# Kernel tuning notes

Measured on AMD Instinct MI355X. Metric: run time of the kernel, lower is better.

The kernel has to match this reference:

```python
import jax, jax.numpy as jnp
import numpy as np

NUM_HEADS = 8
EPS = 1e-12  # torch F.normalize eps

def _conv(x, w, padding, groups=1):
    return jax.lax.conv_general_dilated(
        x, w, window_strides=(1, 1), padding=padding,
        dimension_numbers=('NCHW', 'OIHW', 'NCHW'),
        feature_group_count=groups)

def setup_inputs() -> dict:
    key = jax.random.key(0)
    ks = jax.random.split(key, 5)
    b, dim, h, w = 8, 192, 128, 128
    kv = jax.random.normal(ks[0], (b, dim, h, w), dtype=jnp.float32)
    q = jax.random.normal(ks[1], (b, dim, h, w), dtype=jnp.float32)
    qkv1_w = jax.random.normal(ks[2], (2 * dim, dim, 1, 1), dtype=jnp.float32) * (1.0 / np.sqrt(dim))
    qkv2_w = jax.random.normal(ks[3], (2 * dim, 1, 3, 3), dtype=jnp.float32) * (1.0 / 3.0)
    proj_w = jax.random.normal(ks[4], (dim, dim, 1, 1), dtype=jnp.float32) * (1.0 / np.sqrt(dim))
    scale = jnp.ones((NUM_HEADS, 1, 1), dtype=jnp.float32)
    return {"kv": kv, "q": q, "qkv1_w": qkv1_w, "qkv2_w": qkv2_w,
            "proj_w": proj_w, "scale": scale}

def reference(kv, q, qkv1_w, qkv2_w, proj_w, scale):
    b, c, h, w = kv.shape
    head = NUM_HEADS
    cd = c // head  # channels per head
    hw = h * w
    # 1x1 conv dim -> 2*dim, then 3x3 depthwise conv (groups = 2*dim)
    kv_f = _conv(kv, qkv1_w, padding='VALID')
    kv_f = _conv(kv_f, qkv2_w, padding=((1, 1), (1, 1)), groups=2 * c)
    k, v = jnp.split(kv_f, 2, axis=1)
    # rearrange to [b, head, c, hw]
    qh = q.reshape(b, head, cd, hw)
    kh = k.reshape(b, head, cd, hw)
    vh = v.reshape(b, head, cd, hw)
    # L2-normalize along spatial dim (torch F.normalize semantics)
    qh = qh / jnp.maximum(jnp.linalg.norm(qh, axis=-1, keepdims=True), EPS)
    kh = kh / jnp.maximum(jnp.linalg.norm(kh, axis=-1, keepdims=True), EPS)
    # channel attention: [b, head, c, c]
    attn = jnp.einsum('bhcn,bhdn->bhcd', qh, kh) * scale  # scale broadcasts [head,1,1]
    attn = jax.nn.softmax(attn, axis=-1)
    out = jnp.einsum('bhcd,bhdn->bhcn', attn, vh)  # [b, head, c, hw]
    out = out.reshape(b, c, h, w)
    out = _conv(out, proj_w, padding='VALID')
    return out
```

## Files before the change

kernel.cpp:

```cpp
#include <hip/hip_runtime.h>
#include <hip/hip_bf16.h>

#define HW 16384
#define DIM 192
#define DIM2 384
#define NB 8
#define HEADS 8
#define CD 24
#define NSPLIT 64

typedef float f32x4 __attribute__((ext_vector_type(4)));
typedef short bf16x8 __attribute__((ext_vector_type(8)));
typedef short s16x4 __attribute__((ext_vector_type(4)));

__device__ __forceinline__ short f2bf(float f) {
    __hip_bfloat16 h = __float2bfloat16(f);
    return *reinterpret_cast<short*>(&h);
}
__device__ __forceinline__ float bf2f(short s) {
    __hip_bfloat16 h = *reinterpret_cast<__hip_bfloat16*>(&s);
    return __bfloat162float(h);
}

__global__ __launch_bounds__(256)
void prep_w1(const float* __restrict__ w1, short* __restrict__ wb1)
{
    int idx = blockIdx.x * 256 + threadIdx.x;
    if (idx >= 9216) return;
    int mi = idx / 384, rem = idx % 384;
    int c = rem >> 6, l = rem & 63;
    int oc = mi * 16 + (l & 15);
    int kb = c * 32 + (l >> 4) * 8;
    const float* src = w1 + (long)oc * DIM + kb;
    float4 v0 = *reinterpret_cast<const float4*>(src);
    float4 v1 = *reinterpret_cast<const float4*>(src + 4);
    bf16x8 o;
    o[0]=f2bf(v0.x); o[1]=f2bf(v0.y); o[2]=f2bf(v0.z); o[3]=f2bf(v0.w);
    o[4]=f2bf(v1.x); o[5]=f2bf(v1.y); o[6]=f2bf(v1.z); o[7]=f2bf(v1.w);
    *reinterpret_cast<bf16x8*>(wb1 + (long)idx * 8) = o;
}

template<int NOCT, bool B_F32, bool PER_BATCH_A, bool OUT_F32>
__global__ __launch_bounds__(256, 2)
void gemm_k192(const short* __restrict__ Ab, const void* __restrict__ Bg,
               void* __restrict__ Cg, long bstrideB, long bstrideC)
{
    __shared__ short lds[128 * 200];
    __shared__ float eps[4][16 * 36];
    const int tid  = threadIdx.x;
    const int lane = tid & 63;
    const int wave = tid >> 6;
    const int pxbase = blockIdx.x * 256;
    const int b    = blockIdx.y;

    const int row  = lane & 15;
    const int kgrp = lane >> 4;
    const short* A0 = Ab + (PER_BATCH_A ? (long)b * NOCT * 3072 : 0);

    bf16x8 aA[6], aB[6];
    auto loadA = [&](bf16x8* dst, int mi) {
#pragma unroll
        for (int c = 0; c < 6; c++)
            dst[c] = *reinterpret_cast<const bf16x8*>(
                &A0[((long)(mi * 6 + c) * 64 + lane) * 8]);
    };

    const int q  = tid & 31;
    const int kl = tid >> 5;
    f32x4 stf[6][4];
    s16x4 sth[6][4];
    auto SLOAD = [&](int px0) {
        if constexpr (B_F32) {
            const float* src = (const float*)Bg + (long)b * bstrideB + px0 + q * 4;
#pragma unroll
            for (int j = 0; j < 6; j++)
#pragma unroll
                for (int e = 0; e < 4; e++)
                    stf[j][e] = __builtin_nontemporal_load(
                        reinterpret_cast<const f32x4*>(src + (long)(32 * j + 4 * kl + e) * HW));
        } else {
            const short* src = (const short*)Bg + (long)b * bstrideB + px0 + q * 4;
#pragma unroll
            for (int j = 0; j < 6; j++)
#pragma unroll
                for (int e = 0; e < 4; e++)
                    sth[j][e] = __builtin_nontemporal_load(
                        reinterpret_cast<const s16x4*>(src + (long)(32 * j + 4 * kl + e) * HW));
        }
    };
    auto SWRITE = [&]() {
        const int goff = (((kl >> 1) ^ (q & 3)) << 3) + (kl & 1) * 4;
#pragma unroll
        for (int j = 0; j < 6; j++) {
#pragma unroll
            for (int i = 0; i < 4; i++) {
                s16x4 t;
                if constexpr (B_F32)
                    t = (s16x4){f2bf(stf[j][0][i]), f2bf(stf[j][1][i]),
                                f2bf(stf[j][2][i]), f2bf(stf[j][3][i])};
                else
                    t = (s16x4){sth[j][0][i], sth[j][1][i], sth[j][2][i], sth[j][3][i]};
                *(s16x4*)&lds[(q * 4 + i) * 200 + 32 * j + goff] = t;
            }
        }
    };

    bf16x8 bv[2][6];
    auto HOIST = [&]() {
        const int bro = wave * 32 + row;
        const int sgr = (row >> 2) & 3;
#pragma unroll
        for (int c = 0; c < 6; c++) {
            bv[0][c] = *(const bf16x8*)&lds[bro * 200 + c * 32 + ((kgrp ^ sgr) << 3)];
            bv[1][c] = *(const bf16x8*)&lds[(bro + 16) * 200 + c * 32 + ((kgrp ^ sgr) << 3)];
        }
    };

    const int ocl = lane >> 2;
    float* ep = &eps[wave][0];
    auto computeStore = [&](const bf16x8* a, int mi, int px0) {
        f32x4 acc0 = (f32x4){0.f, 0.f, 0.f, 0.f};
        f32x4 acc1 = (f32x4){0.f, 0.f, 0.f, 0.f};
#pragma unroll
        for (int c = 0; c < 6; c++) {
            acc0 = __builtin_amdgcn_mfma_f32_16x16x32_bf16(a[c], bv[0][c], acc0, 0, 0, 0);
            acc1 = __builtin_amdgcn_mfma_f32_16x16x32_bf16(a[c], bv[1][c], acc1, 0, 0, 0);
        }
#pragma unroll
        for (int r = 0; r < 4; r++) {
            ep[(kgrp * 4 + r) * 36 + row]      = acc0[r];
            ep[(kgrp * 4 + r) * 36 + 16 + row] = acc1[r];
        }
#pragma unroll
        for (int t = 0; t < 2; t++) {
            const int pxq = (lane & 3) + t * 4;
            f32x4 vv = *reinterpret_cast<const f32x4*>(&ep[ocl * 36 + pxq * 4]);
            long off = (long)b * bstrideC + (long)(mi * 16 + ocl) * HW
                     + px0 + wave * 32 + pxq * 4;
            if constexpr (OUT_F32) {
                __builtin_nontemporal_store(vv, reinterpret_cast<f32x4*>((float*)Cg + off));
            } else {
                *reinterpret_cast<s16x4*>((short*)Cg + off) =
                    (s16x4){f2bf(vv[0]), f2bf(vv[1]), f2bf(vv[2]), f2bf(vv[3])};
            }
        }
    };
    auto COMPUTE = [&](int px0) {
        for (int mi = 0; mi < NOCT; mi += 2) {
            loadA(aB, mi + 1);
            computeStore(aA, mi, px0);
            if (mi + 2 < NOCT) loadA(aA, mi + 2);
            computeStore(aB, mi + 1, px0);
        }
    };

    loadA(aA, 0);
    SLOAD(pxbase);
    SWRITE();
    __syncthreads();
    HOIST();
    __syncthreads();
    SLOAD(pxbase + 128);
    COMPUTE(pxbase);
    loadA(aA, 0);
    SWRITE();
    __syncthreads();
    HOIST();
    COMPUTE(pxbase + 128);
}

__global__ __launch_bounds__(256)
void dwconv_sumsq(const short* __restrict__ in, const float* __restrict__ w2,
                  short* __restrict__ outp, float* __restrict__ kss)
{
    __shared__ float red[4];
    const long bgc = blockIdx.x;
    const int  gc  = (int)(bgc % DIM2);
    const int  b   = (int)(bgc / DIM2);
    const int  tid = threadIdx.x;
    const int  tx  = tid & 15;
    const int  ty  = tid >> 4;
    const int  lane = tid & 63;
    const int  x0 = tx * 8;
    const int  y0 = ty * 8;
    const short* src = in + (bgc << 14);
    short* dst = outp + (bgc << 14);

    float w[9];
#pragma unroll
    for (int i = 0; i < 9; i++) w[i] = w2[gc * 9 + i];

    float r0[10], r1[10], r2[10];
    auto loadRow = [&](float* r, int y) {
        if ((unsigned)y > 127u) {
#pragma unroll
            for (int i = 0; i < 10; i++) r[i] = 0.f;
            return;
        }
        bf16x8 v = *reinterpret_cast<const bf16x8*>(&src[y * 128 + x0]);
#pragma unroll
        for (int i = 0; i < 8; i++) r[i + 1] = bf2f(v[i]);
        float left  = __shfl(r[8], lane - 1);
        float right = __shfl(r[1], lane + 1);
        r[0] = (tx == 0)  ? 0.f : left;
        r[9] = (tx == 15) ? 0.f : right;
    };

    loadRow(r0, y0 - 1);
    loadRow(r1, y0);
    float ssq = 0.f;
#pragma unroll
    for (int k = 0; k < 8; k++) {
        const int yy = y0 + k;
        loadRow(r2, yy + 1);
        bf16x8 o;
#pragma unroll
        for (int j = 0; j < 8; j++) {
            float s = r0[j] * w[0] + r0[j + 1] * w[1] + r0[j + 2] * w[2]
                    + r1[j] * w[3] + r1[j + 1] * w[4] + r1[j + 2] * w[5]
                    + r2[j] * w[6] + r2[j + 1] * w[7] + r2[j + 2] * w[8];
            o[j] = f2bf(s);
            ssq += s * s;
        }
        *reinterpret_cast<bf16x8*>(&dst[yy * 128 + x0]) = o;
#pragma unroll
        for (int i = 0; i < 10; i++) { r0[i] = r1[i]; r1[i] = r2[i]; }
    }

    for (int o = 32; o; o >>= 1) ssq += __shfl_xor(ssq, o);
    if ((tid & 63) == 0) red[tid >> 6] = ssq;
    __syncthreads();
    if (gc < DIM && tid == 0)
        kss[b * DIM + gc] = red[0] + red[1] + red[2] + red[3];
}

__global__ __launch_bounds__(64)
void qk_mfma(const float* __restrict__ q, const short* __restrict__ kvb,
             float* __restrict__ part, float* __restrict__ pssq)
{
    const int split = blockIdx.x;
    const int bh    = blockIdx.y;
    const int b = bh >> 3, h = bh & 7;
    const int lane = threadIdx.x;
    const int row = lane & 15;
    const int kg  = (lane >> 4) * 8;
    const int CHUNK = HW / NSPLIT;

    const int qr1 = min(h * CD + 16 + row, DIM - 1);
    const float* q0 = q + ((long)b * DIM + h * CD + row) * HW + split * CHUNK + kg;
    const float* q1 = q + ((long)b * DIM + qr1) * HW + split * CHUNK + kg;
    const short* k0 = kvb + ((long)b * DIM2 + h * CD + row) * HW + split * CHUNK + kg;
    const short* k1 = k0 + 16L * HW;

    f32x4 acc[2][2];
#pragma unroll
    for (int m = 0; m < 2; m++)
#pragma unroll
        for (int n = 0; n < 2; n++) acc[m][n] = (f32x4){0.f, 0.f, 0.f, 0.f};
    float ssq0 = 0.f, ssq1 = 0.f;

#pragma unroll
    for (int s = 0; s < CHUNK / 32; s++) {
        const int px = s * 32;
        float4 qa = *reinterpret_cast<const float4*>(q0 + px);
        float4 qb = *reinterpret_cast<const float4*>(q0 + px + 4);
        float4 qc = *reinterpret_cast<const float4*>(q1 + px);
        float4 qd = *reinterpret_cast<const float4*>(q1 + px + 4);
        bf16x8 b0 = *reinterpret_cast<const bf16x8*>(k0 + px);
        bf16x8 b1 = *reinterpret_cast<const bf16x8*>(k1 + px);
        ssq0 += qa.x*qa.x + qa.y*qa.y + qa.z*qa.z + qa.w*qa.w
              + qb.x*qb.x + qb.y*qb.y + qb.z*qb.z + qb.w*qb.w;
        ssq1 += qc.x*qc.x + qc.y*qc.y + qc.z*qc.z + qc.w*qc.w
              + qd.x*qd.x + qd.y*qd.y + qd.z*qd.z + qd.w*qd.w;
        bf16x8 a0, a1;
        a0[0]=f2bf(qa.x); a0[1]=f2bf(qa.y); a0[2]=f2bf(qa.z); a0[3]=f2bf(qa.w);
        a0[4]=f2bf(qb.x); a0[5]=f2bf(qb.y); a0[6]=f2bf(qb.z); a0[7]=f2bf(qb.w);
        a1[0]=f2bf(qc.x); a1[1]=f2bf(qc.y); a1[2]=f2bf(qc.z); a1[3]=f2bf(qc.w);
        a1[4]=f2bf(qd.x); a1[5]=f2bf(qd.y); a1[6]=f2bf(qd.z); a1[7]=f2bf(qd.w);
        acc[0][0] = __builtin_amdgcn_mfma_f32_16x16x32_bf16(a0, b0, acc[0][0], 0, 0, 0);
        acc[0][1] = __builtin_amdgcn_mfma_f32_16x16x32_bf16(a0, b1, acc[0][1], 0, 0, 0);
        acc[1][0] = __builtin_amdgcn_mfma_f32_16x16x32_bf16(a1, b0, acc[1][0], 0, 0, 0);
        acc[1][1] = __builtin_amdgcn_mfma_f32_16x16x32_bf16(a1, b1, acc[1][1], 0, 0, 0);
    }

    ssq0 += __shfl_xor(ssq0, 16); ssq0 += __shfl_xor(ssq0, 32);
    ssq1 += __shfl_xor(ssq1, 16); ssq1 += __shfl_xor(ssq1, 32);

    float* pd = part + ((long)split * 64 + bh) * 576;
#pragma unroll
    for (int m = 0; m < 2; m++)
#pragma unroll
        for (int n = 0; n < 2; n++)
#pragma unroll
            for (int r = 0; r < 4; r++) {
                int c = m * 16 + (lane >> 4) * 4 + r;
                int d = n * 16 + row;
                if (c < CD && d < CD) pd[c * CD + d] = acc[m][n][r];
            }
    if (lane < 16) {
        float* ps = pssq + ((long)split * 64 + bh) * 32;
        ps[lane]      = ssq0;
        ps[16 + lane] = ssq1;
    }
}

__global__ __launch_bounds__(64)
void softmax_kernel(const float* __restrict__ part, const float* __restrict__ pssq,
                    const float* __restrict__ kss, const float* __restrict__ scale,
                    float* __restrict__ prob)
{
    const int blk = blockIdx.x;
    const int b = blk / DIM;
    const int hc = blk % DIM;
    const int h = hc / CD, c = hc % CD;
    const int bh = b * 8 + h;
    const int d = threadIdx.x;

    float qs = 0.f;
    for (int s = 0; s < NSPLIT; s++) qs += pssq[((long)s * 64 + bh) * 32 + c];

    float val = -1e30f;
    if (d < CD) {
        float raw = 0.f;
        for (int s = 0; s < NSPLIT; s++) raw += part[((long)s * 64 + bh) * 576 + c * CD + d];
        float qn = fmaxf(sqrtf(qs), 1e-12f);
        float kn = fmaxf(sqrtf(kss[b * DIM + h * CD + d]), 1e-12f);
        val = raw * scale[h] / (qn * kn);
    }
    float m = val;
    for (int o = 32; o; o >>= 1) m = fmaxf(m, __shfl_xor(m, o));
    float e = (d < CD) ? expf(val - m) : 0.f;
    float s = e;
    for (int o = 32; o; o >>= 1) s += __shfl_xor(s, o);
    if (d < CD) prob[(long)blk * CD + d] = e / s;
}

__global__ __launch_bounds__(256)
void buildm(const float* __restrict__ pw, const float* __restrict__ prob,
            short* __restrict__ M)
{
    int idx = blockIdx.x * 256 + threadIdx.x;
    if (idx >= 36864) return;
    int b   = idx / 4608, rem = idx % 4608;
    int mi  = rem / 384, r2 = rem % 384;
    int c   = r2 >> 6, l = r2 & 63;
    int oc  = mi * 16 + (l & 15);
    int gb  = c * 32 + (l >> 4) * 8;
    bf16x8 o;
#pragma unroll
    for (int e = 0; e < 8; e++) {
        int gvc = gb + e;
        int h = gvc / CD, d = gvc % CD;
        float s = 0.f;
#pragma unroll
        for (int cc = 0; cc < CD; cc++)
            s += pw[oc * DIM + h * CD + cc] * prob[((long)b * DIM + h * CD + cc) * CD + d];
        o[e] = f2bf(s);
    }
    *reinterpret_cast<bf16x8*>(M + (long)idx * 8) = o;
}

extern "C" void kernel_launch(void* const* d_in, const int* in_sizes, int n_in,
                              void* d_out, int out_size, void* d_ws, size_t ws_size,
                              hipStream_t stream)
{
    const float* kv    = (const float*)d_in[0];
    const float* q     = (const float*)d_in[1];
    const float* w1    = (const float*)d_in[2];
    const float* w2    = (const float*)d_in[3];
    const float* pw    = (const float*)d_in[4];
    const float* scale = (const float*)d_in[5];
    float* out = (float*)d_out;

    char* ws = (char*)d_ws;
    long off = 0;
    auto alloc = [&](long bytes) { char* p = ws + off; off += (bytes + 255) & ~255L; return p; };
    short* kvf1 = (short*)alloc((long)NB * DIM2 * HW * 2);
    short* kvb  = (short*)alloc((long)NB * DIM2 * HW * 2);
    short* wb1  = (short*)alloc((long)DIM2 * DIM * 2);
    float* kss  = (float*)alloc((long)NB * DIM * 4);
    float* part = (float*)alloc((long)NSPLIT * 64 * 576 * 4);
    float* pssq = (float*)alloc((long)NSPLIT * 64 * 32 * 4);
    float* prob = (float*)alloc((long)64 * 576 * 4);
    short* M    = (short*)alloc((long)NB * DIM * DIM * 2);

    prep_w1<<<36, 256, 0, stream>>>(w1, wb1);

    gemm_k192<24, true, false, false><<<dim3(64, NB), 256, 0, stream>>>(
        wb1, kv, kvf1, (long)DIM * HW, (long)DIM2 * HW);

    dwconv_sumsq<<<NB * DIM2, 256, 0, stream>>>(kvf1, w2, kvb, kss);

    qk_mfma<<<dim3(NSPLIT, 64), 64, 0, stream>>>(q, kvb, part, pssq);

    softmax_kernel<<<NB * DIM, 64, 0, stream>>>(part, pssq, kss, scale, prob);

    buildm<<<144, 256, 0, stream>>>(pw, prob, M);

    gemm_k192<12, false, true, true><<<dim3(64, NB), 256, 0, stream>>>(
        M, kvb + (long)DIM * HW, out, (long)DIM2 * HW, (long)DIM * HW);
}
```

Baseline: 179.4 us.

## Interleave next-tile B staging loads and LDS writes with current-tile MFMA compute

The monolithic load and LDS-write of the second pixel tile is split into six per-chunk steps. These are spread across the output-channel loop of the first tile's compute, with at most three chunks in flight at a time. This hides global-load latency behind MFMA work and cuts the number of staging registers live during compute, which may allow better occupancy or less spilling. It depends on NOCT being large enough that every chunk gets written before the barrier. The interleaving also adds extra work inside the compute loop.

```diff
diff --git a/kernel.cpp b/kernel.cpp
--- a/kernel.cpp
+++ b/kernel.cpp
@@ -69,39 +69,32 @@
     const int kl = tid >> 5;
     f32x4 stf[6][4];
     s16x4 sth[6][4];
-    auto SLOAD = [&](int px0) {
+    auto SLOADJ = [&](int px0, int j) {
         if constexpr (B_F32) {
             const float* src = (const float*)Bg + (long)b * bstrideB + px0 + q * 4;
 #pragma unroll
-            for (int j = 0; j < 6; j++)
-#pragma unroll
-                for (int e = 0; e < 4; e++)
-                    stf[j][e] = __builtin_nontemporal_load(
-                        reinterpret_cast<const f32x4*>(src + (long)(32 * j + 4 * kl + e) * HW));
+            for (int e = 0; e < 4; e++)
+                stf[j][e] = __builtin_nontemporal_load(
+                    reinterpret_cast<const f32x4*>(src + (long)(32 * j + 4 * kl + e) * HW));
         } else {
             const short* src = (const short*)Bg + (long)b * bstrideB + px0 + q * 4;
 #pragma unroll
-            for (int j = 0; j < 6; j++)
-#pragma unroll
-                for (int e = 0; e < 4; e++)
-                    sth[j][e] = __builtin_nontemporal_load(
-                        reinterpret_cast<const s16x4*>(src + (long)(32 * j + 4 * kl + e) * HW));
-        }
-    };
-    auto SWRITE = [&]() {
+            for (int e = 0; e < 4; e++)
+                sth[j][e] = __builtin_nontemporal_load(
+                    reinterpret_cast<const s16x4*>(src + (long)(32 * j + 4 * kl + e) * HW));
+        }
+    };
+    auto SWRITEJ = [&](int j) {
         const int goff = (((kl >> 1) ^ (q & 3)) << 3) + (kl & 1) * 4;
 #pragma unroll
-        for (int j = 0; j < 6; j++) {
-#pragma unroll
-            for (int i = 0; i < 4; i++) {
-                s16x4 t;
-                if constexpr (B_F32)
-                    t = (s16x4){f2bf(stf[j][0][i]), f2bf(stf[j][1][i]),
-                                f2bf(stf[j][2][i]), f2bf(stf[j][3][i])};
-                else
-                    t = (s16x4){sth[j][0][i], sth[j][1][i], sth[j][2][i], sth[j][3][i]};
-                *(s16x4*)&lds[(q * 4 + i) * 200 + 32 * j + goff] = t;
-            }
+        for (int i = 0; i < 4; i++) {
+            s16x4 t;
+            if constexpr (B_F32)
+                t = (s16x4){f2bf(stf[j][0][i]), f2bf(stf[j][1][i]),
+                            f2bf(stf[j][2][i]), f2bf(stf[j][3][i])};
+            else
+                t = (s16x4){sth[j][0][i], sth[j][1][i], sth[j][2][i], sth[j][3][i]};
+            *(s16x4*)&lds[(q * 4 + i) * 200 + 32 * j + goff] = t;
         }
     };
 
@@ -145,28 +138,39 @@
             }
         }
     };
-    auto COMPUTE = [&](int px0) {
-        for (int mi = 0; mi < NOCT; mi += 2) {
-            loadA(aB, mi + 1);
-            computeStore(aA, mi, px0);
-            if (mi + 2 < NOCT) loadA(aA, mi + 2);
-            computeStore(aB, mi + 1, px0);
-        }
-    };
 
     loadA(aA, 0);
-    SLOAD(pxbase);
-    SWRITE();
+    SLOADJ(pxbase, 0); SLOADJ(pxbase, 1); SLOADJ(pxbase, 2);
+    SWRITEJ(0); SLOADJ(pxbase, 3);
+    SWRITEJ(1); SLOADJ(pxbase, 4);
+    SWRITEJ(2); SLOADJ(pxbase, 5);
+    SWRITEJ(3); SWRITEJ(4); SWRITEJ(5);
     __syncthreads();
     HOIST();
     __syncthreads();
-    SLOAD(pxbase + 128);
-    COMPUTE(pxbase);
+
+    SLOADJ(pxbase + 128, 0); SLOADJ(pxbase + 128, 1); SLOADJ(pxbase + 128, 2);
+#pragma unroll
+    for (int mi = 0; mi < NOCT; mi += 2) {
+        loadA(aB, mi + 1);
+        computeStore(aA, mi, pxbase);
+        if (mi + 2 < NOCT) loadA(aA, mi + 2);
+        const int p = mi >> 1;
+        if (p < 3) SLOADJ(pxbase + 128, p + 3);
+        if (p < 6) SWRITEJ(p);
+        computeStore(aB, mi + 1, pxbase);
+    }
     loadA(aA, 0);
-    SWRITE();
     __syncthreads();
     HOIST();
-    COMPUTE(pxbase + 128);
+
+#pragma unroll
+    for (int mi = 0; mi < NOCT; mi += 2) {
+        loadA(aB, mi + 1);
+        computeStore(aA, mi, pxbase + 128);
+        if (mi + 2 < NOCT) loadA(aA, mi + 2);
+        computeStore(aB, mi + 1, pxbase + 128);
+    }
 }
 
 __global__ __launch_bounds__(256)
```

New measurement: 201.2 us. 1.12x slower.
